# Optimization experiments

Measured on AMD Instinct MI355X. Metric: run time of the kernel, lower is better.

## Reference

```python
import jax, jax.numpy as jnp
import numpy as np

K = 3
EPS = 1e-16

def setup_inputs() -> dict:
    key = jax.random.key(0)
    k1, k2, k3 = jax.random.split(key, 3)
    x = jax.random.normal(k1, (4096, 256), dtype=jnp.float32)
    pos_l = jax.random.normal(k2, (4096, 3), dtype=jnp.float32)
    pos_h = jax.random.normal(k3, (16384, 3), dtype=jnp.float32)
    return {"x": x, "pos_l": pos_l, "pos_h": pos_h}

def reference(x, pos_l, pos_h):
    # Squared pairwise distances [N_h, N_l] via expansion (GEMM-friendly)
    d2 = (jnp.sum(pos_h * pos_h, axis=1)[:, None]
          - 2.0 * pos_h @ pos_l.T
          + jnp.sum(pos_l * pos_l, axis=1)[None, :])
    # k nearest coarse neighbors per fine point
    _, idx = jax.lax.top_k(-d2, K)                      # idx: [N_h, K]
    # Recompute exact squared distances for selected neighbors (matches PyG knn_interpolate)
    diff = pos_h[:, None, :] - pos_l[idx]               # [N_h, K, D]
    d2_sel = jnp.sum(diff * diff, axis=-1)              # [N_h, K]
    w = 1.0 / jnp.clip(d2_sel, EPS)                     # inverse-distance weights
    feats = x[idx]                                      # [N_h, K, F]
    y = jnp.sum(feats * w[:, :, None], axis=1) / jnp.sum(w, axis=1, keepdims=True)
    return y
```

## Files before the change

### kernel.cpp

```cpp
#include <hip/hip_runtime.h>
#include <math.h>

#define NL    4096
#define NH    16384
#define NF4   64
#define BLK   1024
#define NW    16
#define FPB   64
#define PERW  (NL / NW)
#define BATCH 16

typedef float v16f __attribute__((ext_vector_type(16)));

__device__ __forceinline__ void ins3(float d, int j,
    float& b0, float& b1, float& b2, int& i0, int& i1, int& i2)
{
  const bool p0 = d < b0;
  const bool p1 = d < b1;
  const bool p2 = d < b2;
  const int ni0 = p0 ? j : i0;
  const int ni1 = p0 ? i0 : (p1 ? j : i1);
  const int ni2 = p1 ? i1 : (p2 ? j : i2);
  const float nb0 = fminf(b0, d);
  const float nb1 = __builtin_amdgcn_fmed3f(d, b0, b1);
  const float nb2 = __builtin_amdgcn_fmed3f(d, b1, b2);
  b0 = nb0; b1 = nb1; b2 = nb2;
  i0 = ni0; i1 = ni1; i2 = ni2;
}

__device__ __forceinline__ void lexins3(float d, int j,
    float& b0, float& b1, float& b2, int& i0, int& i1, int& i2)
{
  bool s2 = (d < b2) || ((d == b2) && (j < i2));
  b2 = s2 ? d : b2;  i2 = s2 ? j : i2;
  bool s1 = (b2 < b1) || ((b2 == b1) && (i2 < i1));
  float tf = b1; int ti = i1;
  b1 = s1 ? b2 : b1;  i1 = s1 ? i2 : i1;
  b2 = s1 ? tf : b2;  i2 = s1 ? ti : i2;
  bool s0 = (b1 < b0) || ((b1 == b0) && (i1 < i0));
  tf = b0; ti = i0;
  b0 = s0 ? b1 : b0;  i0 = s0 ? i1 : i0;
  b1 = s0 ? tf : b1;  i1 = s0 ? ti : i1;
}

__device__ __forceinline__ void eval4(const v16f& s, int jb, const float h0,
    const float h1, const float h2, const float hh,
    float& b0, float& b1, float& b2, int& i0, int& i1, int& i2)
{
  #pragma unroll
  for (int i = 0; i < 4; ++i) {
    const float lx = s[i * 4 + 0], ly = s[i * 4 + 1];
    const float lz = s[i * 4 + 2], lw = s[i * 4 + 3];
    const float dot = __fmaf_rn(h2, lz, __fmaf_rn(h1, ly, __fmul_rn(h0, lx)));
    const float d   = __fadd_rn(__fsub_rn(hh, __fmul_rn(2.0f, dot)), lw);
    ins3(d, jb + i, b0, b1, b2, i0, i1, i2);
  }
}

__global__ __launch_bounds__(256)
void prep_kernel(const float* __restrict__ pos_l, float4* __restrict__ cand)
{
  const int i = blockIdx.x * 256 + threadIdx.x;
  const float l0 = pos_l[i * 3 + 0];
  const float l1 = pos_l[i * 3 + 1];
  const float l2 = pos_l[i * 3 + 2];
  const float ll = __fadd_rn(__fadd_rn(__fmul_rn(l0, l0), __fmul_rn(l1, l1)),
                             __fmul_rn(l2, l2));
  cand[i] = make_float4(l0, l1, l2, ll);
}

__global__ __launch_bounds__(BLK)
void knn_interp_kernel(const float* __restrict__ x,
                       const float* __restrict__ pos_l,
                       const float* __restrict__ pos_h,
                       const float* __restrict__ cand,
                       float* __restrict__ out)
{
  __shared__ float  pd[NW * FPB * 3];
  __shared__ int    pj[NW * FPB * 3];
  __shared__ float  wn[FPB * 3];
  __shared__ int    sj[FPB * 3];

  const int tid  = threadIdx.x;
  const int lane = tid & 63;
  const int wv   = __builtin_amdgcn_readfirstlane(tid >> 6);
  const int fg   = blockIdx.x * FPB + lane;

  const float h0 = pos_h[fg * 3 + 0];
  const float h1 = pos_h[fg * 3 + 1];
  const float h2 = pos_h[fg * 3 + 2];
  const float hh = __fadd_rn(__fadd_rn(__fmul_rn(h0, h0), __fmul_rn(h1, h1)),
                             __fmul_rn(h2, h2));

  float a0 = INFINITY, a1 = INFINITY, a2 = INFINITY;  int ai0 = 0, ai1 = 0, ai2 = 0;
  float c0 = INFINITY, c1 = INFINITY, c2 = INFINITY;  int ci0 = 0, ci1 = 0, ci2 = 0;

  const int jbase = __builtin_amdgcn_readfirstlane(wv * PERW);

  for (int t = 0; t < PERW; t += BATCH) {
    v16f sA, sB, sC, sD;
    const float* p = cand + (size_t)(jbase + t) * 4;
    asm volatile("s_load_dwordx16 %0, %4, 0x0\n\t"
                 "s_load_dwordx16 %1, %4, 0x40\n\t"
                 "s_load_dwordx16 %2, %4, 0x80\n\t"
                 "s_load_dwordx16 %3, %4, 0xc0"
                 : "=&s"(sA), "=&s"(sB), "=&s"(sC), "=&s"(sD)
                 : "s"(p));
    asm volatile("s_waitcnt lgkmcnt(0)"
                 : "+s"(sA), "+s"(sB), "+s"(sC), "+s"(sD));

    eval4(sA, jbase + t +  0, h0, h1, h2, hh, a0, a1, a2, ai0, ai1, ai2);
    eval4(sB, jbase + t +  4, h0, h1, h2, hh, a0, a1, a2, ai0, ai1, ai2);
    eval4(sC, jbase + t +  8, h0, h1, h2, hh, c0, c1, c2, ci0, ci1, ci2);
    eval4(sD, jbase + t + 12, h0, h1, h2, hh, c0, c1, c2, ci0, ci1, ci2);
  }

  lexins3(c0, ci0, a0, a1, a2, ai0, ai1, ai2);
  lexins3(c1, ci1, a0, a1, a2, ai0, ai1, ai2);
  lexins3(c2, ci2, a0, a1, a2, ai0, ai1, ai2);

  {
    const int s = (wv * FPB + lane) * 3;
    pd[s + 0] = a0; pd[s + 1] = a1; pd[s + 2] = a2;
    pj[s + 0] = ai0; pj[s + 1] = ai1; pj[s + 2] = ai2;
  }
  __syncthreads();

  if (tid < FPB) {
    float b0 = INFINITY, b1 = INFINITY, b2 = INFINITY;
    int   i0 = 0x7fffffff, i1 = 0x7fffffff, i2 = 0x7fffffff;
    for (int w = 0; w < NW; ++w) {
      const int s = (w * FPB + tid) * 3;
      lexins3(pd[s + 0], pj[s + 0], b0, b1, b2, i0, i1, i2);
      lexins3(pd[s + 1], pj[s + 1], b0, b1, b2, i0, i1, i2);
      lexins3(pd[s + 2], pj[s + 2], b0, b1, b2, i0, i1, i2);
    }

    const int fm = blockIdx.x * FPB + tid;
    const float H0 = pos_h[fm * 3 + 0];
    const float H1 = pos_h[fm * 3 + 1];
    const float H2 = pos_h[fm * 3 + 2];

    float wk[3];
    int   jk[3] = { i0, i1, i2 };
    #pragma unroll
    for (int k = 0; k < 3; ++k) {
      const int j = jk[k];
      const float dx = __fsub_rn(H0, pos_l[j * 3 + 0]);
      const float dy = __fsub_rn(H1, pos_l[j * 3 + 1]);
      const float dz = __fsub_rn(H2, pos_l[j * 3 + 2]);
      float d2 = __fadd_rn(__fadd_rn(__fmul_rn(dx, dx), __fmul_rn(dy, dy)),
                           __fmul_rn(dz, dz));
      d2 = fmaxf(d2, 1e-16f);
      wk[k] = __frcp_rn(d2);
    }
    const float W  = __fadd_rn(__fadd_rn(wk[0], wk[1]), wk[2]);
    const float rW = __frcp_rn(W);
    #pragma unroll
    for (int k = 0; k < 3; ++k) {
      wn[tid * 3 + k] = wk[k] * rW;
      sj[tid * 3 + k] = jk[k];
    }
  }
  __syncthreads();

  const float4* __restrict__ x4   = (const float4*)x;
  float4* __restrict__       out4 = (float4*)out;
  #pragma unroll
  for (int i = 0; i < (FPB * NF4) / BLK; ++i) {
    const int task = tid + i * BLK;
    const int f    = task >> 6;
    const int cc   = task & 63;
    const int j0 = sj[f * 3 + 0], j1 = sj[f * 3 + 1], j2 = sj[f * 3 + 2];
    const float w0 = wn[f * 3 + 0], w1 = wn[f * 3 + 1], w2 = wn[f * 3 + 2];
    const float4 xa = x4[j0 * NF4 + cc];
    const float4 xb = x4[j1 * NF4 + cc];
    const float4 xc = x4[j2 * NF4 + cc];
    float4 r;
    r.x = xa.x * w0 + xb.x * w1 + xc.x * w2;
    r.y = xa.y * w0 + xb.y * w1 + xc.y * w2;
    r.z = xa.z * w0 + xb.z * w1 + xc.z * w2;
    r.w = xa.w * w0 + xb.w * w1 + xc.w * w2;
    out4[(blockIdx.x * FPB + f) * NF4 + cc] = r;
  }
}

extern "C" void kernel_launch(void* const* d_in, const int* in_sizes, int n_in,
                              void* d_out, int out_size, void* d_ws, size_t ws_size,
                              hipStream_t stream)
{
  const float* x     = (const float*)d_in[0];
  const float* pos_l = (const float*)d_in[1];
  const float* pos_h = (const float*)d_in[2];
  float* out = (float*)d_out;
  float* cand = (float*)d_ws;

  hipLaunchKernelGGL(prep_kernel, dim3(NL / 256), dim3(256), 0, stream,
                     pos_l, (float4*)cand);
  hipLaunchKernelGGL(knn_interp_kernel, dim3(NH / FPB), dim3(BLK), 0, stream,
                     x, pos_l, pos_h, cand, out);
}
```

Measured before the change: 108.8 us.

## Split KNN scan across two candidate halves with packed-FP32 SoA distance evaluation

Converts the candidate table to a structure-of-arrays layout and computes two candidate distances per instruction using v_pk_fma_f32 inline assembly. The brute-force scan grid is doubled: each block scans half of the coarse points and writes partial top-3 results to workspace, and a separate finish kernel merges the halves and does the weighted gather. The aim is more blocks for occupancy across CUs plus fewer VALU instructions per candidate. This adds a kernel launch and a global round trip for the partials. The old single-kernel path is kept as a fallback when the workspace is too small.

```diff
diff --git a/kernel.cpp b/kernel.cpp
--- a/kernel.cpp
+++ b/kernel.cpp
@@ -4,13 +4,18 @@
 #define NL    4096
 #define NH    16384
 #define NF4   64
-#define BLK   1024
-#define NW    16
 #define FPB   64
-#define PERW  (NL / NW)
-#define BATCH 16
+
+#define BLKA  1024
+#define NWA   16
+#define NHALF 2048
+#define SLICE 128
+#define BLKF  1024
+#define NWF   16
+#define PERWF (NL / NWF)
 
 typedef float v16f __attribute__((ext_vector_type(16)));
+typedef float v2f  __attribute__((ext_vector_type(2)));
 
 __device__ __forceinline__ void ins3(float d, int j,
     float& b0, float& b1, float& b2, int& i0, int& i1, int& i2)
@@ -43,22 +48,24 @@
   b1 = s0 ? tf : b1;  i1 = s0 ? ti : i1;
 }
 
-__device__ __forceinline__ void eval4(const v16f& s, int jb, const float h0,
-    const float h1, const float h2, const float hh,
-    float& b0, float& b1, float& b2, int& i0, int& i1, int& i2)
-{
-  #pragma unroll
-  for (int i = 0; i < 4; ++i) {
-    const float lx = s[i * 4 + 0], ly = s[i * 4 + 1];
-    const float lz = s[i * 4 + 2], lw = s[i * 4 + 3];
-    const float dot = __fmaf_rn(h2, lz, __fmaf_rn(h1, ly, __fmul_rn(h0, lx)));
-    const float d   = __fadd_rn(__fsub_rn(hh, __fmul_rn(2.0f, dot)), lw);
-    ins3(d, jb + i, b0, b1, b2, i0, i1, i2);
-  }
+__device__ __forceinline__ v2f dist2_pk(v2f lx, v2f ly, v2f lz, v2f ll,
+                                        v2f h00, v2f h11, v2f h22, v2f hhh,
+                                        v2f m22)
+{
+  v2f d;
+  asm("v_pk_mul_f32 %0, %1, %2\n\t"
+      "v_pk_fma_f32 %0, %3, %4, %0\n\t"
+      "v_pk_fma_f32 %0, %5, %6, %0\n\t"
+      "v_pk_fma_f32 %0, %0, %7, %8\n\t"
+      "v_pk_add_f32 %0, %0, %9"
+      : "=&v"(d)
+      : "v"(h00), "s"(lx), "v"(h11), "s"(ly), "v"(h22), "s"(lz),
+        "v"(m22), "v"(hhh), "s"(ll));
+  return d;
 }
 
 __global__ __launch_bounds__(256)
-void prep_kernel(const float* __restrict__ pos_l, float4* __restrict__ cand)
+void prep_soa_kernel(const float* __restrict__ pos_l, float* __restrict__ cand)
 {
   const int i = blockIdx.x * 256 + threadIdx.x;
   const float l0 = pos_l[i * 3 + 0];
@@ -66,53 +73,63 @@
   const float l2 = pos_l[i * 3 + 2];
   const float ll = __fadd_rn(__fadd_rn(__fmul_rn(l0, l0), __fmul_rn(l1, l1)),
                              __fmul_rn(l2, l2));
-  cand[i] = make_float4(l0, l1, l2, ll);
-}
-
-__global__ __launch_bounds__(BLK)
-void knn_interp_kernel(const float* __restrict__ x,
-                       const float* __restrict__ pos_l,
-                       const float* __restrict__ pos_h,
-                       const float* __restrict__ cand,
-                       float* __restrict__ out)
-{
-  __shared__ float  pd[NW * FPB * 3];
-  __shared__ int    pj[NW * FPB * 3];
-  __shared__ float  wn[FPB * 3];
-  __shared__ int    sj[FPB * 3];
+  cand[i]          = l0;
+  cand[NL + i]     = l1;
+  cand[2 * NL + i] = l2;
+  cand[3 * NL + i] = ll;
+}
+
+__global__ __launch_bounds__(BLKA)
+void knn_scan_kernel(const float* __restrict__ pos_h,
+                     const float* __restrict__ cand,
+                     float* __restrict__ pdist,
+                     int*   __restrict__ pidx)
+{
+  __shared__ float pd[NWA * FPB * 3];
+  __shared__ int   pj[NWA * FPB * 3];
 
   const int tid  = threadIdx.x;
   const int lane = tid & 63;
   const int wv   = __builtin_amdgcn_readfirstlane(tid >> 6);
-  const int fg   = blockIdx.x * FPB + lane;
+  const int half = blockIdx.x & 1;
+  const int fgrp = blockIdx.x >> 1;
+  const int fg   = fgrp * FPB + lane;
 
   const float h0 = pos_h[fg * 3 + 0];
   const float h1 = pos_h[fg * 3 + 1];
   const float h2 = pos_h[fg * 3 + 2];
   const float hh = __fadd_rn(__fadd_rn(__fmul_rn(h0, h0), __fmul_rn(h1, h1)),
                              __fmul_rn(h2, h2));
+  const v2f h00 = { h0, h0 }, h11 = { h1, h1 }, h22 = { h2, h2 };
+  const v2f hhh = { hh, hh }, m22 = { -2.0f, -2.0f };
 
   float a0 = INFINITY, a1 = INFINITY, a2 = INFINITY;  int ai0 = 0, ai1 = 0, ai2 = 0;
   float c0 = INFINITY, c1 = INFINITY, c2 = INFINITY;  int ci0 = 0, ci1 = 0, ci2 = 0;
 
-  const int jbase = __builtin_amdgcn_readfirstlane(wv * PERW);
-
-  for (int t = 0; t < PERW; t += BATCH) {
-    v16f sA, sB, sC, sD;
-    const float* p = cand + (size_t)(jbase + t) * 4;
+  const int jbase = __builtin_amdgcn_readfirstlane(half * NHALF + wv * SLICE);
+
+  for (int t = 0; t < SLICE; t += 16) {
+    v16f sx, sy, sz, sw;
+    const float* p = cand + jbase + t;
     asm volatile("s_load_dwordx16 %0, %4, 0x0\n\t"
-                 "s_load_dwordx16 %1, %4, 0x40\n\t"
-                 "s_load_dwordx16 %2, %4, 0x80\n\t"
-                 "s_load_dwordx16 %3, %4, 0xc0"
-                 : "=&s"(sA), "=&s"(sB), "=&s"(sC), "=&s"(sD)
+                 "s_load_dwordx16 %1, %4, 0x4000\n\t"
+                 "s_load_dwordx16 %2, %4, 0x8000\n\t"
+                 "s_load_dwordx16 %3, %4, 0xc000"
+                 : "=&s"(sx), "=&s"(sy), "=&s"(sz), "=&s"(sw)
                  : "s"(p));
     asm volatile("s_waitcnt lgkmcnt(0)"
-                 : "+s"(sA), "+s"(sB), "+s"(sC), "+s"(sD));
-
-    eval4(sA, jbase + t +  0, h0, h1, h2, hh, a0, a1, a2, ai0, ai1, ai2);
-    eval4(sB, jbase + t +  4, h0, h1, h2, hh, a0, a1, a2, ai0, ai1, ai2);
-    eval4(sC, jbase + t +  8, h0, h1, h2, hh, c0, c1, c2, ci0, ci1, ci2);
-    eval4(sD, jbase + t + 12, h0, h1, h2, hh, c0, c1, c2, ci0, ci1, ci2);
+                 : "+s"(sx), "+s"(sy), "+s"(sz), "+s"(sw));
+
+    #pragma unroll
+    for (int pr = 0; pr < 8; ++pr) {
+      const v2f lx = { sx[2 * pr], sx[2 * pr + 1] };
+      const v2f ly = { sy[2 * pr], sy[2 * pr + 1] };
+      const v2f lz = { sz[2 * pr], sz[2 * pr + 1] };
+      const v2f lw = { sw[2 * pr], sw[2 * pr + 1] };
+      const v2f d  = dist2_pk(lx, ly, lz, lw, h00, h11, h22, hhh, m22);
+      ins3(d.x, jbase + t + 2 * pr,     a0, a1, a2, ai0, ai1, ai2);
+      ins3(d.y, jbase + t + 2 * pr + 1, c0, c1, c2, ci0, ci1, ci2);
+    }
   }
 
   lexins3(c0, ci0, a0, a1, a2, ai0, ai1, ai2);
@@ -129,18 +146,43 @@
   if (tid < FPB) {
     float b0 = INFINITY, b1 = INFINITY, b2 = INFINITY;
     int   i0 = 0x7fffffff, i1 = 0x7fffffff, i2 = 0x7fffffff;
-    for (int w = 0; w < NW; ++w) {
+    for (int w = 0; w < NWA; ++w) {
       const int s = (w * FPB + tid) * 3;
       lexins3(pd[s + 0], pj[s + 0], b0, b1, b2, i0, i1, i2);
       lexins3(pd[s + 1], pj[s + 1], b0, b1, b2, i0, i1, i2);
       lexins3(pd[s + 2], pj[s + 2], b0, b1, b2, i0, i1, i2);
     }
-
-    const int fm = blockIdx.x * FPB + tid;
-    const float H0 = pos_h[fm * 3 + 0];
-    const float H1 = pos_h[fm * 3 + 1];
-    const float H2 = pos_h[fm * 3 + 2];
-
+    const int o = (half * NH + fgrp * FPB + tid) * 3;
+    pdist[o + 0] = b0; pdist[o + 1] = b1; pdist[o + 2] = b2;
+    pidx[o + 0]  = i0; pidx[o + 1]  = i1; pidx[o + 2]  = i2;
+  }
+}
+
+__global__ __launch_bounds__(1024)
+void knn_finish_kernel(const float* __restrict__ x,
+                       const float* __restrict__ pos_l,
+                       const float* __restrict__ pos_h,
+                       const float* __restrict__ pdist,
+                       const int*   __restrict__ pidx,
+                       float* __restrict__ out)
+{
+  __shared__ float wn[FPB * 3];
+  __shared__ int   sj[FPB * 3];
+  const int tid = threadIdx.x;
+
+  if (tid < FPB) {
+    const int f  = blockIdx.x * FPB + tid;
+    const int o0 = f * 3;
+    const int o1 = (NH + f) * 3;
+    float b0 = pdist[o0], b1 = pdist[o0 + 1], b2 = pdist[o0 + 2];
+    int   i0 = pidx[o0],  i1 = pidx[o0 + 1],  i2 = pidx[o0 + 2];
+    lexins3(pdist[o1],     pidx[o1],     b0, b1, b2, i0, i1, i2);
+    lexins3(pdist[o1 + 1], pidx[o1 + 1], b0, b1, b2, i0, i1, i2);
+    lexins3(pdist[o1 + 2], pidx[o1 + 2], b0, b1, b2, i0, i1, i2);
+
+    const float H0 = pos_h[f * 3 + 0];
+    const float H1 = pos_h[f * 3 + 1];
+    const float H2 = pos_h[f * 3 + 2];
     float wk[3];
     int   jk[3] = { i0, i1, i2 };
     #pragma unroll
@@ -167,8 +209,8 @@
   const float4* __restrict__ x4   = (const float4*)x;
   float4* __restrict__       out4 = (float4*)out;
   #pragma unroll
-  for (int i = 0; i < (FPB * NF4) / BLK; ++i) {
-    const int task = tid + i * BLK;
+  for (int i = 0; i < (FPB * NF4) / 1024; ++i) {
+    const int task = tid + i * 1024;
     const int f    = task >> 6;
     const int cc   = task & 63;
     const int j0 = sj[f * 3 + 0], j1 = sj[f * 3 + 1], j2 = sj[f * 3 + 2];
@@ -185,6 +227,145 @@
   }
 }
 
+__global__ __launch_bounds__(256)
+void fb_prep_kernel(const float* __restrict__ pos_l, float4* __restrict__ cand)
+{
+  const int i = blockIdx.x * 256 + threadIdx.x;
+  const float l0 = pos_l[i * 3 + 0];
+  const float l1 = pos_l[i * 3 + 1];
+  const float l2 = pos_l[i * 3 + 2];
+  const float ll = __fadd_rn(__fadd_rn(__fmul_rn(l0, l0), __fmul_rn(l1, l1)),
+                             __fmul_rn(l2, l2));
+  cand[i] = make_float4(l0, l1, l2, ll);
+}
+
+__device__ __forceinline__ void fb_eval4(const v16f& s, int jb, const float h0,
+    const float h1, const float h2, const float hh,
+    float& b0, float& b1, float& b2, int& i0, int& i1, int& i2)
+{
+  #pragma unroll
+  for (int i = 0; i < 4; ++i) {
+    const float lx = s[i * 4 + 0], ly = s[i * 4 + 1];
+    const float lz = s[i * 4 + 2], lw = s[i * 4 + 3];
+    const float dot = __fmaf_rn(h2, lz, __fmaf_rn(h1, ly, __fmul_rn(h0, lx)));
+    const float d   = __fadd_rn(__fsub_rn(hh, __fmul_rn(2.0f, dot)), lw);
+    ins3(d, jb + i, b0, b1, b2, i0, i1, i2);
+  }
+}
+
+__global__ __launch_bounds__(BLKF)
+void fb_knn_kernel(const float* __restrict__ x,
+                   const float* __restrict__ pos_l,
+                   const float* __restrict__ pos_h,
+                   const float* __restrict__ cand,
+                   float* __restrict__ out)
+{
+  __shared__ float  pd[NWF * FPB * 3];
+  __shared__ int    pj[NWF * FPB * 3];
+  __shared__ float  wn[FPB * 3];
+  __shared__ int    sj[FPB * 3];
+
+  const int tid  = threadIdx.x;
+  const int lane = tid & 63;
+  const int wv   = __builtin_amdgcn_readfirstlane(tid >> 6);
+  const int fg   = blockIdx.x * FPB + lane;
+
+  const float h0 = pos_h[fg * 3 + 0];
+  const float h1 = pos_h[fg * 3 + 1];
+  const float h2 = pos_h[fg * 3 + 2];
+  const float hh = __fadd_rn(__fadd_rn(__fmul_rn(h0, h0), __fmul_rn(h1, h1)),
+                             __fmul_rn(h2, h2));
+
+  float a0 = INFINITY, a1 = INFINITY, a2 = INFINITY;  int ai0 = 0, ai1 = 0, ai2 = 0;
+  float c0 = INFINITY, c1 = INFINITY, c2 = INFINITY;  int ci0 = 0, ci1 = 0, ci2 = 0;
+
+  const int jbase = __builtin_amdgcn_readfirstlane(wv * PERWF);
+
+  for (int t = 0; t < PERWF; t += 16) {
+    v16f sA, sB, sC, sD;
+    const float* p = cand + (size_t)(jbase + t) * 4;
+    asm volatile("s_load_dwordx16 %0, %4, 0x0\n\t"
+                 "s_load_dwordx16 %1, %4, 0x40\n\t"
+                 "s_load_dwordx16 %2, %4, 0x80\n\t"
+                 "s_load_dwordx16 %3, %4, 0xc0"
+                 : "=&s"(sA), "=&s"(sB), "=&s"(sC), "=&s"(sD)
+                 : "s"(p));
+    asm volatile("s_waitcnt lgkmcnt(0)"
+                 : "+s"(sA), "+s"(sB), "+s"(sC), "+s"(sD));
+    fb_eval4(sA, jbase + t +  0, h0, h1, h2, hh, a0, a1, a2, ai0, ai1, ai2);
+    fb_eval4(sB, jbase + t +  4, h0, h1, h2, hh, a0, a1, a2, ai0, ai1, ai2);
+    fb_eval4(sC, jbase + t +  8, h0, h1, h2, hh, c0, c1, c2, ci0, ci1, ci2);
+    fb_eval4(sD, jbase + t + 12, h0, h1, h2, hh, c0, c1, c2, ci0, ci1, ci2);
+  }
+
+  lexins3(c0, ci0, a0, a1, a2, ai0, ai1, ai2);
+  lexins3(c1, ci1, a0, a1, a2, ai0, ai1, ai2);
+  lexins3(c2, ci2, a0, a1, a2, ai0, ai1, ai2);
+
+  {
+    const int s = (wv * FPB + lane) * 3;
+    pd[s + 0] = a0; pd[s + 1] = a1; pd[s + 2] = a2;
+    pj[s + 0] = ai0; pj[s + 1] = ai1; pj[s + 2] = ai2;
+  }
+  __syncthreads();
+
+  if (tid < FPB) {
+    float b0 = INFINITY, b1 = INFINITY, b2 = INFINITY;
+    int   i0 = 0x7fffffff, i1 = 0x7fffffff, i2 = 0x7fffffff;
+    for (int w = 0; w < NWF; ++w) {
+      const int s = (w * FPB + tid) * 3;
+      lexins3(pd[s + 0], pj[s + 0], b0, b1, b2, i0, i1, i2);
+      lexins3(pd[s + 1], pj[s + 1], b0, b1, b2, i0, i1, i2);
+      lexins3(pd[s + 2], pj[s + 2], b0, b1, b2, i0, i1, i2);
+    }
+    const int fm = blockIdx.x * FPB + tid;
+    const float H0 = pos_h[fm * 3 + 0];
+    const float H1 = pos_h[fm * 3 + 1];
+    const float H2 = pos_h[fm * 3 + 2];
+    float wk[3];
+    int   jk[3] = { i0, i1, i2 };
+    #pragma unroll
+    for (int k = 0; k < 3; ++k) {
+      const int j = jk[k];
+      const float dx = __fsub_rn(H0, pos_l[j * 3 + 0]);
+      const float dy = __fsub_rn(H1, pos_l[j * 3 + 1]);
+      const float dz = __fsub_rn(H2, pos_l[j * 3 + 2]);
+      float d2 = __fadd_rn(__fadd_rn(__fmul_rn(dx, dx), __fmul_rn(dy, dy)),
+                           __fmul_rn(dz, dz));
+      d2 = fmaxf(d2, 1e-16f);
+      wk[k] = __frcp_rn(d2);
+    }
+    const float W  = __fadd_rn(__fadd_rn(wk[0], wk[1]), wk[2]);
+    const float rW = __frcp_rn(W);
+    #pragma unroll
+    for (int k = 0; k < 3; ++k) {
+      wn[tid * 3 + k] = wk[k] * rW;
+      sj[tid * 3 + k] = jk[k];
+    }
+  }
+  __syncthreads();
+
+  const float4* __restrict__ x4   = (const float4*)x;
+  float4* __restrict__       out4 = (float4*)out;
+  #pragma unroll
+  for (int i = 0; i < (FPB * NF4) / BLKF; ++i) {
+    const int task = tid + i * BLKF;
+    const int f    = task >> 6;
+    const int cc   = task & 63;
+    const int j0 = sj[f * 3 + 0], j1 = sj[f * 3 + 1], j2 = sj[f * 3 + 2];
+    const float w0 = wn[f * 3 + 0], w1 = wn[f * 3 + 1], w2 = wn[f * 3 + 2];
+    const float4 xa = x4[j0 * NF4 + cc];
+    const float4 xb = x4[j1 * NF4 + cc];
+    const float4 xc = x4[j2 * NF4 + cc];
+    float4 r;
+    r.x = xa.x * w0 + xb.x * w1 + xc.x * w2;
+    r.y = xa.y * w0 + xb.y * w1 + xc.y * w2;
+    r.z = xa.z * w0 + xb.z * w1 + xc.z * w2;
+    r.w = xa.w * w0 + xb.w * w1 + xc.w * w2;
+    out4[(blockIdx.x * FPB + f) * NF4 + cc] = r;
+  }
+}
+
 extern "C" void kernel_launch(void* const* d_in, const int* in_sizes, int n_in,
                               void* d_out, int out_size, void* d_ws, size_t ws_size,
                               hipStream_t stream)
@@ -193,10 +374,25 @@
   const float* pos_l = (const float*)d_in[1];
   const float* pos_h = (const float*)d_in[2];
   float* out = (float*)d_out;
-  float* cand = (float*)d_ws;
-
-  hipLaunchKernelGGL(prep_kernel, dim3(NL / 256), dim3(256), 0, stream,
-                     pos_l, (float4*)cand);
-  hipLaunchKernelGGL(knn_interp_kernel, dim3(NH / FPB), dim3(BLK), 0, stream,
-                     x, pos_l, pos_h, cand, out);
-}
+
+  const size_t need = (size_t)(4 * NL) * 4
+                    + (size_t)(2 * NH * 3) * 4 * 2;
+
+  if (ws_size >= need) {
+    float* cand  = (float*)d_ws;
+    float* pdist = cand + 4 * NL;
+    int*   pidx  = (int*)(pdist + 2 * NH * 3);
+    hipLaunchKernelGGL(prep_soa_kernel, dim3(NL / 256), dim3(256), 0, stream,
+                       pos_l, cand);
+    hipLaunchKernelGGL(knn_scan_kernel, dim3((NH / FPB) * 2), dim3(BLKA), 0,
+                       stream, pos_h, cand, pdist, pidx);
+    hipLaunchKernelGGL(knn_finish_kernel, dim3(NH / FPB), dim3(1024), 0,
+                       stream, x, pos_l, pos_h, pdist, pidx, out);
+  } else {
+    float* cand = (float*)d_ws;
+    hipLaunchKernelGGL(fb_prep_kernel, dim3(NL / 256), dim3(256), 0, stream,
+                       pos_l, (float4*)cand);
+    hipLaunchKernelGGL(fb_knn_kernel, dim3(NH / FPB), dim3(BLKF), 0, stream,
+                       x, pos_l, pos_h, cand, out);
+  }
+}
```

After: 115.4 us. 1.06x slower.

## Pack distance and index into sortable uint keys with packed-FP32 distance math

Applied to the files above, without the earlier changes.

Each squared distance is clamped to non-negative and its low 12 mantissa bits are replaced by the candidate index, giving one unsigned key. A top-6 list is then kept with cheap v_min/v_med3_u32 chains instead of separate float and index selects. Distances are computed two candidates at a time with v_pk_fma_f32 on structure-of-arrays candidate data. Because the truncated keys are only approximate, the final top-3 is chosen by recomputing exact distances for the 6 survivors with lexicographic tie-breaking. The risk is that the right neighbors could fall outside the 6 kept keys when several distances are nearly equal.

```diff
diff --git a/kernel.cpp b/kernel.cpp
--- a/kernel.cpp
+++ b/kernel.cpp
@@ -8,24 +8,35 @@
 #define NW    16
 #define FPB   64
 #define PERW  (NL / NW)
-#define BATCH 16
+#define TOPM  6
 
 typedef float v16f __attribute__((ext_vector_type(16)));
-
-__device__ __forceinline__ void ins3(float d, int j,
-    float& b0, float& b1, float& b2, int& i0, int& i1, int& i2)
-{
-  const bool p0 = d < b0;
-  const bool p1 = d < b1;
-  const bool p2 = d < b2;
-  const int ni0 = p0 ? j : i0;
-  const int ni1 = p0 ? i0 : (p1 ? j : i1);
-  const int ni2 = p1 ? i1 : (p2 ? j : i2);
-  const float nb0 = fminf(b0, d);
-  const float nb1 = __builtin_amdgcn_fmed3f(d, b0, b1);
-  const float nb2 = __builtin_amdgcn_fmed3f(d, b1, b2);
-  b0 = nb0; b1 = nb1; b2 = nb2;
-  i0 = ni0; i1 = ni1; i2 = ni2;
+typedef float v2f  __attribute__((ext_vector_type(2)));
+
+__device__ __forceinline__ unsigned int med3u(unsigned int a, unsigned int b,
+                                              unsigned int c)
+{
+  unsigned int d;
+  asm("v_med3_u32 %0, %1, %2, %3" : "=v"(d) : "v"(a), "v"(b), "v"(c));
+  return d;
+}
+__device__ __forceinline__ unsigned int minu(unsigned int a, unsigned int b)
+{
+  unsigned int d;
+  asm("v_min_u32 %0, %1, %2" : "=v"(d) : "v"(a), "v"(b));
+  return d;
+}
+__device__ __forceinline__ void ins6(unsigned int k,
+    unsigned int& b0, unsigned int& b1, unsigned int& b2,
+    unsigned int& b3, unsigned int& b4, unsigned int& b5)
+{
+  const unsigned int n0 = minu(b0, k);
+  const unsigned int n1 = med3u(k, b0, b1);
+  const unsigned int n2 = med3u(k, b1, b2);
+  const unsigned int n3 = med3u(k, b2, b3);
+  const unsigned int n4 = med3u(k, b3, b4);
+  const unsigned int n5 = med3u(k, b4, b5);
+  b0 = n0; b1 = n1; b2 = n2; b3 = n3; b4 = n4; b5 = n5;
 }
 
 __device__ __forceinline__ void lexins3(float d, int j,
@@ -43,22 +54,24 @@
   b1 = s0 ? tf : b1;  i1 = s0 ? ti : i1;
 }
 
-__device__ __forceinline__ void eval4(const v16f& s, int jb, const float h0,
-    const float h1, const float h2, const float hh,
-    float& b0, float& b1, float& b2, int& i0, int& i1, int& i2)
-{
-  #pragma unroll
-  for (int i = 0; i < 4; ++i) {
-    const float lx = s[i * 4 + 0], ly = s[i * 4 + 1];
-    const float lz = s[i * 4 + 2], lw = s[i * 4 + 3];
-    const float dot = __fmaf_rn(h2, lz, __fmaf_rn(h1, ly, __fmul_rn(h0, lx)));
-    const float d   = __fadd_rn(__fsub_rn(hh, __fmul_rn(2.0f, dot)), lw);
-    ins3(d, jb + i, b0, b1, b2, i0, i1, i2);
-  }
+__device__ __forceinline__ v2f dist2_pk(v2f lx, v2f ly, v2f lz, v2f ll,
+                                        v2f h00, v2f h11, v2f h22, v2f hhh,
+                                        v2f m22)
+{
+  v2f d;
+  asm("v_pk_mul_f32 %0, %1, %2\n\t"
+      "v_pk_fma_f32 %0, %3, %4, %0\n\t"
+      "v_pk_fma_f32 %0, %5, %6, %0\n\t"
+      "v_pk_fma_f32 %0, %0, %7, %8\n\t"
+      "v_pk_add_f32 %0, %0, %9"
+      : "=&v"(d)
+      : "v"(h00), "s"(lx), "v"(h11), "s"(ly), "v"(h22), "s"(lz),
+        "v"(m22), "v"(hhh), "s"(ll));
+  return d;
 }
 
 __global__ __launch_bounds__(256)
-void prep_kernel(const float* __restrict__ pos_l, float4* __restrict__ cand)
+void prep_soa_kernel(const float* __restrict__ pos_l, float* __restrict__ cand)
 {
   const int i = blockIdx.x * 256 + threadIdx.x;
   const float l0 = pos_l[i * 3 + 0];
@@ -66,7 +79,10 @@
   const float l2 = pos_l[i * 3 + 2];
   const float ll = __fadd_rn(__fadd_rn(__fmul_rn(l0, l0), __fmul_rn(l1, l1)),
                              __fmul_rn(l2, l2));
-  cand[i] = make_float4(l0, l1, l2, ll);
+  cand[i]          = l0;
+  cand[NL + i]     = l1;
+  cand[2 * NL + i] = l2;
+  cand[3 * NL + i] = ll;
 }
 
 __global__ __launch_bounds__(BLK)
@@ -76,10 +92,9 @@
                        const float* __restrict__ cand,
                        float* __restrict__ out)
 {
-  __shared__ float  pd[NW * FPB * 3];
-  __shared__ int    pj[NW * FPB * 3];
-  __shared__ float  wn[FPB * 3];
-  __shared__ int    sj[FPB * 3];
+  __shared__ unsigned int pk_[NW * FPB * TOPM];
+  __shared__ float wn[FPB * 3];
+  __shared__ int   sj[FPB * 3];
 
   const int tid  = threadIdx.x;
   const int lane = tid & 63;
@@ -91,56 +106,93 @@
   const float h2 = pos_h[fg * 3 + 2];
   const float hh = __fadd_rn(__fadd_rn(__fmul_rn(h0, h0), __fmul_rn(h1, h1)),
                              __fmul_rn(h2, h2));
-
-  float a0 = INFINITY, a1 = INFINITY, a2 = INFINITY;  int ai0 = 0, ai1 = 0, ai2 = 0;
-  float c0 = INFINITY, c1 = INFINITY, c2 = INFINITY;  int ci0 = 0, ci1 = 0, ci2 = 0;
+  const v2f h00 = { h0, h0 }, h11 = { h1, h1 }, h22 = { h2, h2 };
+  const v2f hhh = { hh, hh }, m22 = { -2.0f, -2.0f };
+
+  unsigned int kmaskv;
+  asm("v_mov_b32 %0, 0xfffff000" : "=v"(kmaskv));
+
+  unsigned int a0 = ~0u, a1 = ~0u, a2 = ~0u, a3 = ~0u, a4 = ~0u, a5 = ~0u;
+  unsigned int c0 = ~0u, c1 = ~0u, c2 = ~0u, c3 = ~0u, c4 = ~0u, c5 = ~0u;
 
   const int jbase = __builtin_amdgcn_readfirstlane(wv * PERW);
 
-  for (int t = 0; t < PERW; t += BATCH) {
-    v16f sA, sB, sC, sD;
-    const float* p = cand + (size_t)(jbase + t) * 4;
+  for (int t = 0; t < PERW; t += 16) {
+    v16f sx, sy, sz, sw;
+    const float* p = cand + jbase + t;
     asm volatile("s_load_dwordx16 %0, %4, 0x0\n\t"
-                 "s_load_dwordx16 %1, %4, 0x40\n\t"
-                 "s_load_dwordx16 %2, %4, 0x80\n\t"
-                 "s_load_dwordx16 %3, %4, 0xc0"
-                 : "=&s"(sA), "=&s"(sB), "=&s"(sC), "=&s"(sD)
+                 "s_load_dwordx16 %1, %4, 0x4000\n\t"
+                 "s_load_dwordx16 %2, %4, 0x8000\n\t"
+                 "s_load_dwordx16 %3, %4, 0xc000"
+                 : "=&s"(sx), "=&s"(sy), "=&s"(sz), "=&s"(sw)
                  : "s"(p));
     asm volatile("s_waitcnt lgkmcnt(0)"
-                 : "+s"(sA), "+s"(sB), "+s"(sC), "+s"(sD));
-
-    eval4(sA, jbase + t +  0, h0, h1, h2, hh, a0, a1, a2, ai0, ai1, ai2);
-    eval4(sB, jbase + t +  4, h0, h1, h2, hh, a0, a1, a2, ai0, ai1, ai2);
-    eval4(sC, jbase + t +  8, h0, h1, h2, hh, c0, c1, c2, ci0, ci1, ci2);
-    eval4(sD, jbase + t + 12, h0, h1, h2, hh, c0, c1, c2, ci0, ci1, ci2);
-  }
-
-  lexins3(c0, ci0, a0, a1, a2, ai0, ai1, ai2);
-  lexins3(c1, ci1, a0, a1, a2, ai0, ai1, ai2);
-  lexins3(c2, ci2, a0, a1, a2, ai0, ai1, ai2);
+                 : "+s"(sx), "+s"(sy), "+s"(sz), "+s"(sw));
+
+    #pragma unroll
+    for (int pr = 0; pr < 8; ++pr) {
+      const v2f lx = { sx[2 * pr], sx[2 * pr + 1] };
+      const v2f ly = { sy[2 * pr], sy[2 * pr + 1] };
+      const v2f lz = { sz[2 * pr], sz[2 * pr + 1] };
+      const v2f lw = { sw[2 * pr], sw[2 * pr + 1] };
+      const v2f d  = dist2_pk(lx, ly, lz, lw, h00, h11, h22, hhh, m22);
+      const float dx0 = fmaxf(d.x, 0.0f);
+      const float dy0 = fmaxf(d.y, 0.0f);
+      const int j0 = jbase + t + 2 * pr;
+      const int j1 = j0 + 1;
+      unsigned int k0, k1;
+      asm("v_and_or_b32 %0, %1, %2, %3"
+          : "=v"(k0) : "v"(dx0), "v"(kmaskv), "s"(j0));
+      asm("v_and_or_b32 %0, %1, %2, %3"
+          : "=v"(k1) : "v"(dy0), "v"(kmaskv), "s"(j1));
+      ins6(k0, a0, a1, a2, a3, a4, a5);
+      ins6(k1, c0, c1, c2, c3, c4, c5);
+    }
+  }
+
+  ins6(c0, a0, a1, a2, a3, a4, a5);
+  ins6(c1, a0, a1, a2, a3, a4, a5);
+  ins6(c2, a0, a1, a2, a3, a4, a5);
+  ins6(c3, a0, a1, a2, a3, a4, a5);
+  ins6(c4, a0, a1, a2, a3, a4, a5);
+  ins6(c5, a0, a1, a2, a3, a4, a5);
 
   {
-    const int s = (wv * FPB + lane) * 3;
-    pd[s + 0] = a0; pd[s + 1] = a1; pd[s + 2] = a2;
-    pj[s + 0] = ai0; pj[s + 1] = ai1; pj[s + 2] = ai2;
+    const int s = (wv * FPB + lane) * TOPM;
+    pk_[s + 0] = a0; pk_[s + 1] = a1; pk_[s + 2] = a2;
+    pk_[s + 3] = a3; pk_[s + 4] = a4; pk_[s + 5] = a5;
   }
   __syncthreads();
 
   if (tid < FPB) {
-    float b0 = INFINITY, b1 = INFINITY, b2 = INFINITY;
+    unsigned int m0 = ~0u, m1 = ~0u, m2 = ~0u, m3 = ~0u, m4 = ~0u, m5 = ~0u;
+    for (int w = 0; w < NW; ++w) {
+      const int s = (w * FPB + tid) * TOPM;
+      #pragma unroll
+      for (int q = 0; q < TOPM; ++q)
+        ins6(pk_[s + q], m0, m1, m2, m3, m4, m5);
+    }
+
+    const float b_hh = hh;
+    float e0 = INFINITY, e1 = INFINITY, e2 = INFINITY;
     int   i0 = 0x7fffffff, i1 = 0x7fffffff, i2 = 0x7fffffff;
-    for (int w = 0; w < NW; ++w) {
-      const int s = (w * FPB + tid) * 3;
-      lexins3(pd[s + 0], pj[s + 0], b0, b1, b2, i0, i1, i2);
-      lexins3(pd[s + 1], pj[s + 1], b0, b1, b2, i0, i1, i2);
-      lexins3(pd[s + 2], pj[s + 2], b0, b1, b2, i0, i1, i2);
+    const unsigned int mk[TOPM] = { m0, m1, m2, m3, m4, m5 };
+    #pragma unroll
+    for (int q = 0; q < TOPM; ++q) {
+      const int j = (int)(mk[q] & 0xFFFu);
+      const float lx = cand[j];
+      const float ly = cand[NL + j];
+      const float lz = cand[2 * NL + j];
+      const float ll = cand[3 * NL + j];
+      const float dot = __fmaf_rn(h2, lz, __fmaf_rn(h1, ly, __fmul_rn(h0, lx)));
+      const float d2  = __fadd_rn(__fsub_rn(b_hh, __fmul_rn(2.0f, dot)), ll);
+      lexins3(d2, j, e0, e1, e2, i0, i1, i2);
     }
 
     const int fm = blockIdx.x * FPB + tid;
     const float H0 = pos_h[fm * 3 + 0];
     const float H1 = pos_h[fm * 3 + 1];
     const float H2 = pos_h[fm * 3 + 2];
-
     float wk[3];
     int   jk[3] = { i0, i1, i2 };
     #pragma unroll
@@ -192,11 +244,11 @@
   const float* x     = (const float*)d_in[0];
   const float* pos_l = (const float*)d_in[1];
   const float* pos_h = (const float*)d_in[2];
-  float* out = (float*)d_out;
+  float* out  = (float*)d_out;
   float* cand = (float*)d_ws;
 
-  hipLaunchKernelGGL(prep_kernel, dim3(NL / 256), dim3(256), 0, stream,
-                     pos_l, (float4*)cand);
+  hipLaunchKernelGGL(prep_soa_kernel, dim3(NL / 256), dim3(256), 0, stream,
+                     pos_l, cand);
   hipLaunchKernelGGL(knn_interp_kernel, dim3(NH / FPB), dim3(BLK), 0, stream,
                      x, pos_l, pos_h, cand, out);
 }
```

Result: faster. 99.38 us (-8.6%).
